# Kernel tuning notes

Hardware: AMD Instinct MI355X
Metric: run time of the kernel (lower is better)

Reference implementation:

```python
import jax, jax.numpy as jnp
import numpy as np

T, H, I, E = 512, 2048, 1408, 16
G, TOPK_GROUP, TOP_K = 4, 2, 6
RSF = 2.5  # routed_scaling_factor


def setup_inputs() -> dict:
    key = jax.random.key(0)
    ks = jax.random.split(key, 6)
    s = jnp.float32(0.02)
    return {
        "hidden_states": jax.random.normal(ks[0], (T, H), jnp.float32),
        "gate_weight": jax.random.normal(ks[1], (E, H), jnp.float32) * s,
        "correction_bias": jax.random.normal(ks[2], (E,), jnp.float32) * s,
        "w_gate": jax.random.normal(ks[3], (E, I, H), jnp.float32) * s,
        "w_up": jax.random.normal(ks[4], (E, I, H), jnp.float32) * s,
        "w_down": jax.random.normal(ks[5], (E, H, I), jnp.float32) * s,
    }


def _route(x, gate_weight, correction_bias):
    # MoEGate: logits = x @ W^T ; noaux_tc biased grouped top-k (sigmoid scoring)
    logits = x @ gate_weight.T                       # [T, E]
    scores = jax.nn.sigmoid(logits)                  # [T, E]
    sfc = scores + correction_bias                   # scores used for selection only
    # group score = sum of top-2 biased scores within each group
    gs = sfc.reshape(-1, G, E // G)                  # [T, G, E/G]
    group_scores = jax.lax.top_k(gs, 2)[0].sum(-1)   # [T, G]
    gidx = jax.lax.top_k(group_scores, TOPK_GROUP)[1]        # [T, topk_group]
    gmask = jnp.sum(jax.nn.one_hot(gidx, G, dtype=x.dtype), axis=1)  # [T, G]
    emask = jnp.repeat(gmask, E // G, axis=1)        # [T, E]
    masked = jnp.where(emask > 0, sfc, -jnp.inf)
    topk_idx = jax.lax.top_k(masked, TOP_K)[1]       # [T, K]
    # weights come from the UNbiased sigmoid scores
    topk_w = jnp.take_along_axis(scores, topk_idx, axis=1)   # [T, K]
    topk_w = topk_w / jnp.sum(topk_w, axis=-1, keepdims=True)  # renormalize
    topk_w = topk_w * jnp.asarray(RSF, x.dtype)      # routed_scaling_factor
    return topk_w, topk_idx


def _moe(x, topk_w, topk_idx, w_gate, w_up, w_down):
    # dispatch/grouped-GEMM/combine, expressed as a scan over experts with
    # per-token combine coefficients (same math as gather/grouped-GEMM/scatter)
    def step(acc, ws):
        wg, wu, wd, e = ws
        h = jax.nn.silu(x @ wg.T) * (x @ wu.T)       # [T, I] SiluAndMul
        out_e = h @ wd.T                             # [T, H]
        coef = jnp.sum(jnp.where(topk_idx == e, topk_w, 0.0), axis=1)  # [T]
        return acc + coef[:, None] * out_e, None

    acc0 = jnp.zeros_like(x)
    acc, _ = jax.lax.scan(step, acc0, (w_gate, w_up, w_down, jnp.arange(E)))
    return acc


def reference(hidden_states, gate_weight, correction_bias, w_gate, w_up, w_down):
    topk_w, topk_idx = _route(hidden_states, gate_weight, correction_bias)
    return _moe(hidden_states, topk_w, topk_idx, w_gate, w_up, w_down)
```

## Files before the change

### kernel.cpp

```cpp
#include <hip/hip_runtime.h>
#include <cstdint>

#define T_TOK 512
#define H_DIM 2048
#define I_DIM 1408
#define N_EXP 16

typedef __attribute__((ext_vector_type(8))) _Float16 f16x8;
typedef __attribute__((ext_vector_type(4))) float f32x4;

__device__ __forceinline__ void gload_lds16(const void* g, void* l) {
  auto gp = (const __attribute__((address_space(1))) unsigned int*)(unsigned long long)g;
  unsigned int loff = (unsigned int)(unsigned long long)l;
  auto lp = (__attribute__((address_space(3))) unsigned int*)loff;
  __builtin_amdgcn_global_load_lds(gp, lp, 16, 0, 0);
}

__device__ __forceinline__ f16x8 cvt8(f32x4 a, f32x4 b) {
  f16x8 r;
  r[0] = (_Float16)a[0]; r[1] = (_Float16)a[1]; r[2] = (_Float16)a[2]; r[3] = (_Float16)a[3];
  r[4] = (_Float16)b[0]; r[5] = (_Float16)b[1]; r[6] = (_Float16)b[2]; r[7] = (_Float16)b[3];
  return r;
}

__global__ __launch_bounds__(256) void route_kernel(
    const float* __restrict__ x, const float* __restrict__ gw,
    const float* __restrict__ bias, float* __restrict__ coef,
    _Float16* __restrict__ xb) {
  const int t = blockIdx.x;
  const int tid = threadIdx.x;
  const float* xt = x + (size_t)t * H_DIM;
  _Float16* xbt = xb + (size_t)t * H_DIM;

  float part[N_EXP];
#pragma unroll
  for (int e = 0; e < N_EXP; ++e) part[e] = 0.f;
  for (int j = tid; j < H_DIM; j += 256) {
    float xv = xt[j];
    xbt[j] = (_Float16)xv;
#pragma unroll
    for (int e = 0; e < N_EXP; ++e) part[e] += xv * gw[e * H_DIM + j];
  }
#pragma unroll
  for (int e = 0; e < N_EXP; ++e) {
#pragma unroll
    for (int off = 32; off > 0; off >>= 1) part[e] += __shfl_down(part[e], off);
  }
  __shared__ float red[4][N_EXP];
  const int lane = tid & 63, w = tid >> 6;
  if (lane == 0) {
#pragma unroll
    for (int e = 0; e < N_EXP; ++e) red[w][e] = part[e];
  }
  __syncthreads();
  if (tid == 0) {
    float s[16], sf[16];
    for (int e = 0; e < 16; ++e) {
      float lg = red[0][e] + red[1][e] + red[2][e] + red[3][e];
      s[e] = 1.f / (1.f + expf(-lg));
      sf[e] = s[e] + bias[e];
    }
    float gsc[4];
    for (int g = 0; g < 4; ++g) {
      float m1 = -1e30f, m2 = -1e30f;
      for (int j = 0; j < 4; ++j) {
        float v = sf[g * 4 + j];
        if (v > m1) { m2 = m1; m1 = v; }
        else if (v > m2) { m2 = v; }
      }
      gsc[g] = m1 + m2;
    }
    int g1 = 0;
    for (int g = 1; g < 4; ++g) if (gsc[g] > gsc[g1]) g1 = g;
    int g2 = -1;
    for (int g = 0; g < 4; ++g) {
      if (g == g1) continue;
      if (g2 < 0 || gsc[g] > gsc[g2]) g2 = g;
    }
    bool gok[4];
    for (int g = 0; g < 4; ++g) gok[g] = (g == g1) || (g == g2);
    bool sel[16];
    for (int e = 0; e < 16; ++e) sel[e] = false;
    float wsum = 0.f;
    for (int k = 0; k < 6; ++k) {
      int best = -1; float bv = 0.f;
      for (int e2 = 0; e2 < 16; ++e2) {
        if (!gok[e2 >> 2] || sel[e2]) continue;
        if (best < 0 || sf[e2] > bv) { bv = sf[e2]; best = e2; }
      }
      sel[best] = true;
      wsum += s[best];
    }
    float inv = 2.5f / wsum;
    for (int e = 0; e < 16; ++e) coef[t * N_EXP + e] = sel[e] ? s[e] * inv : 0.f;
  }
}

__global__ __launch_bounds__(512) void build_lists_kernel(
    const float* __restrict__ coef, int* __restrict__ counts,
    int* __restrict__ lists) {
  const int e = blockIdx.x;
  const int t = threadIdx.x;
  const bool flag = coef[t * N_EXP + e] != 0.f;
  const unsigned long long m = __ballot(flag);
  const int lane = t & 63, w = t >> 6;
  __shared__ int wcnt[8], woff[8];
  if (lane == 0) wcnt[w] = __popcll(m);
  __syncthreads();
  if (t == 0) {
    int a = 0;
    for (int i = 0; i < 8; ++i) { woff[i] = a; a += wcnt[i]; }
    counts[e] = a;
  }
  __syncthreads();
  if (flag) {
    int pos = woff[w] + __popcll(m & ((1ull << lane) - 1ull));
    lists[e * T_TOK + pos] = t;
  }
}

__global__ __launch_bounds__(512) void gate_up_kernel(
    const _Float16* __restrict__ xb, const float* __restrict__ wg,
    const float* __restrict__ wu, const int* __restrict__ counts,
    const int* __restrict__ lists, _Float16* __restrict__ hbuf) {
  extern __shared__ char lds[];
  const int e = blockIdx.z;
  const int ne = counts[e];
  const int row0 = blockIdx.y * 256;
  if (row0 >= ne) return;
  const int col0 = blockIdx.x * 64;
  const int tid = threadIdx.x;
  const int lane = tid & 63;
  const int w = tid >> 6;
  const int wr = w >> 1, wc = w & 1;

  const int* lst = lists + e * T_TOK;
  const _Float16* asrc[4];
#pragma unroll
  for (int i = 0; i < 4; ++i) {
    int tr = (w * 4 + i) * 8 + (lane >> 3);
    int tok = lst[min(row0 + tr, ne - 1)];
    int lchunk = (lane & 7) ^ (tr & 7);
    asrc[i] = xb + (size_t)tok * H_DIM + lchunk * 8;
  }
  const float* bgs[2];
  const float* bus[2];
#pragma unroll
  for (int i = 0; i < 2; ++i) {
    int tr = (w * 2 + i) * 4 + (lane >> 4);
    int ls = (lane & 15) ^ ((tr & 7) << 1);
    bgs[i] = wg + ((size_t)e * I_DIM + col0 + tr) * H_DIM + ls * 4;
    bus[i] = wu + ((size_t)e * I_DIM + col0 + tr) * H_DIM + ls * 4;
  }

  f32x4 accg[4][2], accu[4][2];
  const f32x4 zz = {0.f, 0.f, 0.f, 0.f};
#pragma unroll
  for (int m = 0; m < 4; ++m)
#pragma unroll
    for (int n = 0; n < 2; ++n) { accg[m][n] = zz; accu[m][n] = zz; }

  auto stage = [&](int kt, int buf) {
    const int k0 = kt * 64;
#pragma unroll
    for (int i = 0; i < 4; ++i)
      gload_lds16(asrc[i] + k0, lds + buf * 32768 + (w * 4 + i) * 1024);
#pragma unroll
    for (int i = 0; i < 2; ++i) {
      gload_lds16(bgs[i] + k0, lds + 65536 + buf * 16384 + (w * 2 + i) * 1024);
      gload_lds16(bus[i] + k0, lds + 98304 + buf * 16384 + (w * 2 + i) * 1024);
    }
  };

  auto comp = [&](int buf) {
    const char* Ab = lds + buf * 32768;
    const char* Gb = lds + 65536 + buf * 16384;
    const char* Ub = lds + 98304 + buf * 16384;
#pragma unroll
    for (int kk = 0; kk < 2; ++kk) {
      f16x8 afr[4], bg[2], bu[2];
#pragma unroll
      for (int m = 0; m < 4; ++m) {
        int row = wr * 64 + m * 16 + (lane & 15);
        int pch = (kk * 4 + (lane >> 4)) ^ (row & 7);
        afr[m] = *(const f16x8*)(Ab + row * 128 + pch * 16);
      }
#pragma unroll
      for (int n = 0; n < 2; ++n) {
        int c = wc * 32 + n * 16 + (lane & 15);
        int s0 = kk * 8 + (lane >> 4) * 2;
        int p0 = s0 ^ ((c & 7) << 1);
        int p1 = (s0 + 1) ^ ((c & 7) << 1);
        bg[n] = cvt8(*(const f32x4*)(Gb + c * 256 + p0 * 16),
                     *(const f32x4*)(Gb + c * 256 + p1 * 16));
        bu[n] = cvt8(*(const f32x4*)(Ub + c * 256 + p0 * 16),
                     *(const f32x4*)(Ub + c * 256 + p1 * 16));
      }
#pragma unroll
      for (int m = 0; m < 4; ++m)
#pragma unroll
        for (int n = 0; n < 2; ++n) {
          accg[m][n] = __builtin_amdgcn_mfma_f32_16x16x32_f16(afr[m], bg[n], accg[m][n], 0, 0, 0);
          accu[m][n] = __builtin_amdgcn_mfma_f32_16x16x32_f16(afr[m], bu[n], accu[m][n], 0, 0, 0);
        }
    }
  };

  const int NK = H_DIM / 64;
  stage(0, 0);
  for (int kt = 0; kt < NK; ++kt) {
    __syncthreads();
    if (kt + 1 < NK) stage(kt + 1, (kt + 1) & 1);
    comp(kt & 1);
  }

  _Float16* hb = hbuf + (size_t)e * T_TOK * I_DIM;
#pragma unroll
  for (int m = 0; m < 4; ++m) {
#pragma unroll
    for (int j = 0; j < 4; ++j) {
      int r = row0 + wr * 64 + m * 16 + (lane >> 4) * 4 + j;
      if (r < ne) {
#pragma unroll
        for (int n = 0; n < 2; ++n) {
          int cc = col0 + wc * 32 + n * 16 + (lane & 15);
          float g = accg[m][n][j];
          float u = accu[m][n][j];
          float hv = (g / (1.f + __expf(-g))) * u;
          hb[(size_t)r * I_DIM + cc] = (_Float16)hv;
        }
      }
    }
  }
}

__global__ __launch_bounds__(512) void down_kernel(
    const _Float16* __restrict__ hbuf, const float* __restrict__ wd,
    const int* __restrict__ counts, const int* __restrict__ lists,
    const float* __restrict__ coef, float* __restrict__ out) {
  extern __shared__ char lds[];
  const int e = blockIdx.z;
  const int ne = counts[e];
  const int row0 = blockIdx.y * 256;
  if (row0 >= ne) return;
  const int col0 = blockIdx.x * 64;
  const int tid = threadIdx.x;
  const int lane = tid & 63;
  const int w = tid >> 6;
  const int wr = w >> 1, wc = w & 1;

  const _Float16* hb = hbuf + (size_t)e * T_TOK * I_DIM;
  const _Float16* asrc[4];
#pragma unroll
  for (int i = 0; i < 4; ++i) {
    int tr = (w * 4 + i) * 8 + (lane >> 3);
    int lchunk = (lane & 7) ^ (tr & 7);
    asrc[i] = hb + (size_t)(row0 + tr) * I_DIM + lchunk * 8;
  }
  const float* bds[2];
#pragma unroll
  for (int i = 0; i < 2; ++i) {
    int tr = (w * 2 + i) * 4 + (lane >> 4);
    int ls = (lane & 15) ^ ((tr & 7) << 1);
    bds[i] = wd + ((size_t)e * H_DIM + col0 + tr) * I_DIM + ls * 4;
  }

  f32x4 acc[4][2];
  const f32x4 zz = {0.f, 0.f, 0.f, 0.f};
#pragma unroll
  for (int m = 0; m < 4; ++m)
#pragma unroll
    for (int n = 0; n < 2; ++n) acc[m][n] = zz;

  auto stage = [&](int kt, int buf) {
    const int k0 = kt * 64;
#pragma unroll
    for (int i = 0; i < 4; ++i)
      gload_lds16(asrc[i] + k0, lds + buf * 32768 + (w * 4 + i) * 1024);
#pragma unroll
    for (int i = 0; i < 2; ++i)
      gload_lds16(bds[i] + k0, lds + 65536 + buf * 16384 + (w * 2 + i) * 1024);
  };

  auto comp = [&](int buf) {
    const char* Ab = lds + buf * 32768;
    const char* Bb = lds + 65536 + buf * 16384;
#pragma unroll
    for (int kk = 0; kk < 2; ++kk) {
      f16x8 afr[4], bf[2];
#pragma unroll
      for (int m = 0; m < 4; ++m) {
        int row = wr * 64 + m * 16 + (lane & 15);
        int pch = (kk * 4 + (lane >> 4)) ^ (row & 7);
        afr[m] = *(const f16x8*)(Ab + row * 128 + pch * 16);
      }
#pragma unroll
      for (int n = 0; n < 2; ++n) {
        int c = wc * 32 + n * 16 + (lane & 15);
        int s0 = kk * 8 + (lane >> 4) * 2;
        int p0 = s0 ^ ((c & 7) << 1);
        int p1 = (s0 + 1) ^ ((c & 7) << 1);
        bf[n] = cvt8(*(const f32x4*)(Bb + c * 256 + p0 * 16),
                     *(const f32x4*)(Bb + c * 256 + p1 * 16));
      }
#pragma unroll
      for (int m = 0; m < 4; ++m)
#pragma unroll
        for (int n = 0; n < 2; ++n)
          acc[m][n] = __builtin_amdgcn_mfma_f32_16x16x32_f16(afr[m], bf[n], acc[m][n], 0, 0, 0);
    }
  };

  const int NK = I_DIM / 64;
  stage(0, 0);
  for (int kt = 0; kt < NK; ++kt) {
    __syncthreads();
    if (kt + 1 < NK) stage(kt + 1, (kt + 1) & 1);
    comp(kt & 1);
  }

#pragma unroll
  for (int m = 0; m < 4; ++m) {
#pragma unroll
    for (int j = 0; j < 4; ++j) {
      int r = row0 + wr * 64 + m * 16 + (lane >> 4) * 4 + j;
      if (r < ne) {
        int tok = lists[e * T_TOK + r];
        float c = coef[tok * N_EXP + e];
#pragma unroll
        for (int n = 0; n < 2; ++n) {
          int cc = col0 + wc * 32 + n * 16 + (lane & 15);
          atomicAdd(&out[(size_t)tok * H_DIM + cc], acc[m][n][j] * c);
        }
      }
    }
  }
}

extern "C" void kernel_launch(void* const* d_in, const int* in_sizes, int n_in,
                              void* d_out, int out_size, void* d_ws, size_t ws_size,
                              hipStream_t stream) {
  const float* x  = (const float*)d_in[0];
  const float* gw = (const float*)d_in[1];
  const float* cb = (const float*)d_in[2];
  const float* wg = (const float*)d_in[3];
  const float* wu = (const float*)d_in[4];
  const float* wd = (const float*)d_in[5];
  float* out = (float*)d_out;
  char* ws = (char*)d_ws;

  float* coef   = (float*)(ws);
  int*   counts = (int*)(ws + 32768);
  int*   lists  = (int*)(ws + 33024);
  _Float16* xb  = (_Float16*)(ws + 66048);
  _Float16* hbuf= (_Float16*)(ws + 66048 + 2097152 + 256);

  hipFuncSetAttribute((const void*)gate_up_kernel,
                      hipFuncAttributeMaxDynamicSharedMemorySize, 131072);
  hipFuncSetAttribute((const void*)down_kernel,
                      hipFuncAttributeMaxDynamicSharedMemorySize, 98304);

  hipMemsetAsync(d_out, 0, (size_t)out_size * sizeof(float), stream);

  route_kernel<<<T_TOK, 256, 0, stream>>>(x, gw, cb, coef, xb);
  build_lists_kernel<<<N_EXP, 512, 0, stream>>>(coef, counts, lists);
  gate_up_kernel<<<dim3(I_DIM / 64, 2, N_EXP), 512, 131072, stream>>>(xb, wg, wu, counts, lists, hbuf);
  down_kernel<<<dim3(H_DIM / 64, 2, N_EXP), 512, 98304, stream>>>(hbuf, wd, counts, lists, coef, out);
}
```

Baseline: 213.1 us.

## Shrink gate_up tile to 128 rows and K=32 with static LDS

```diff
diff --git a/kernel.cpp b/kernel.cpp
--- a/kernel.cpp
+++ b/kernel.cpp
@@ -119,14 +119,14 @@
   }
 }
 
-__global__ __launch_bounds__(512) void gate_up_kernel(
+__global__ __launch_bounds__(256) void gate_up_kernel(
     const _Float16* __restrict__ xb, const float* __restrict__ wg,
     const float* __restrict__ wu, const int* __restrict__ counts,
     const int* __restrict__ lists, _Float16* __restrict__ hbuf) {
-  extern __shared__ char lds[];
+  __shared__ char lds[49152];
   const int e = blockIdx.z;
   const int ne = counts[e];
-  const int row0 = blockIdx.y * 256;
+  const int row0 = blockIdx.y * 128;
   if (row0 >= ne) return;
   const int col0 = blockIdx.x * 64;
   const int tid = threadIdx.x;
@@ -135,20 +135,19 @@
   const int wr = w >> 1, wc = w & 1;
 
   const int* lst = lists + e * T_TOK;
-  const _Float16* asrc[4];
-#pragma unroll
-  for (int i = 0; i < 4; ++i) {
-    int tr = (w * 4 + i) * 8 + (lane >> 3);
-    int tok = lst[min(row0 + tr, ne - 1)];
-    int lchunk = (lane & 7) ^ (tr & 7);
-    asrc[i] = xb + (size_t)tok * H_DIM + lchunk * 8;
+  const _Float16* asrc[2];
+#pragma unroll
+  for (int i = 0; i < 2; ++i) {
+    int r = row0 + (2 * w + i) * 16 + (lane & 15);
+    int tok = lst[min(r, ne - 1)];
+    asrc[i] = xb + (size_t)tok * H_DIM + (lane >> 4) * 8;
   }
   const float* bgs[2];
   const float* bus[2];
 #pragma unroll
   for (int i = 0; i < 2; ++i) {
-    int tr = (w * 2 + i) * 4 + (lane >> 4);
-    int ls = (lane & 15) ^ ((tr & 7) << 1);
+    int tr = (w * 2 + i) * 8 + (lane >> 3);
+    int ls = (lane & 7) ^ (tr & 7);
     bgs[i] = wg + ((size_t)e * I_DIM + col0 + tr) * H_DIM + ls * 4;
     bus[i] = wu + ((size_t)e * I_DIM + col0 + tr) * H_DIM + ls * 4;
   }
@@ -161,52 +160,46 @@
     for (int n = 0; n < 2; ++n) { accg[m][n] = zz; accu[m][n] = zz; }
 
   auto stage = [&](int kt, int buf) {
-    const int k0 = kt * 64;
-#pragma unroll
-    for (int i = 0; i < 4; ++i)
-      gload_lds16(asrc[i] + k0, lds + buf * 32768 + (w * 4 + i) * 1024);
+    const int k0 = kt * 32;
+#pragma unroll
+    for (int i = 0; i < 2; ++i)
+      gload_lds16(asrc[i] + k0, lds + buf * 8192 + (2 * w + i) * 1024);
 #pragma unroll
     for (int i = 0; i < 2; ++i) {
-      gload_lds16(bgs[i] + k0, lds + 65536 + buf * 16384 + (w * 2 + i) * 1024);
-      gload_lds16(bus[i] + k0, lds + 98304 + buf * 16384 + (w * 2 + i) * 1024);
+      gload_lds16(bgs[i] + k0, lds + 16384 + buf * 8192 + (w * 2 + i) * 1024);
+      gload_lds16(bus[i] + k0, lds + 32768 + buf * 8192 + (w * 2 + i) * 1024);
     }
   };
 
   auto comp = [&](int buf) {
-    const char* Ab = lds + buf * 32768;
-    const char* Gb = lds + 65536 + buf * 16384;
-    const char* Ub = lds + 98304 + buf * 16384;
-#pragma unroll
-    for (int kk = 0; kk < 2; ++kk) {
-      f16x8 afr[4], bg[2], bu[2];
-#pragma unroll
-      for (int m = 0; m < 4; ++m) {
-        int row = wr * 64 + m * 16 + (lane & 15);
-        int pch = (kk * 4 + (lane >> 4)) ^ (row & 7);
-        afr[m] = *(const f16x8*)(Ab + row * 128 + pch * 16);
-      }
+    const char* Ab = lds + buf * 8192;
+    const char* Gb = lds + 16384 + buf * 8192;
+    const char* Ub = lds + 32768 + buf * 8192;
+    f16x8 afr[4], bg[2], bu[2];
+#pragma unroll
+    for (int m = 0; m < 4; ++m)
+      afr[m] = *(const f16x8*)(Ab + (wr * 4 + m) * 1024 + lane * 16);
+    const int s0 = (lane >> 4) * 2;
+#pragma unroll
+    for (int n = 0; n < 2; ++n) {
+      int c = wc * 32 + n * 16 + (lane & 15);
+      int p0 = s0 ^ (c & 7);
+      int p1 = (s0 + 1) ^ (c & 7);
+      bg[n] = cvt8(*(const f32x4*)(Gb + c * 128 + p0 * 16),
+                   *(const f32x4*)(Gb + c * 128 + p1 * 16));
+      bu[n] = cvt8(*(const f32x4*)(Ub + c * 128 + p0 * 16),
+                   *(const f32x4*)(Ub + c * 128 + p1 * 16));
+    }
+#pragma unroll
+    for (int m = 0; m < 4; ++m)
 #pragma unroll
       for (int n = 0; n < 2; ++n) {
-        int c = wc * 32 + n * 16 + (lane & 15);
-        int s0 = kk * 8 + (lane >> 4) * 2;
-        int p0 = s0 ^ ((c & 7) << 1);
-        int p1 = (s0 + 1) ^ ((c & 7) << 1);
-        bg[n] = cvt8(*(const f32x4*)(Gb + c * 256 + p0 * 16),
-                     *(const f32x4*)(Gb + c * 256 + p1 * 16));
-        bu[n] = cvt8(*(const f32x4*)(Ub + c * 256 + p0 * 16),
-                     *(const f32x4*)(Ub + c * 256 + p1 * 16));
-      }
-#pragma unroll
-      for (int m = 0; m < 4; ++m)
-#pragma unroll
-        for (int n = 0; n < 2; ++n) {
-          accg[m][n] = __builtin_amdgcn_mfma_f32_16x16x32_f16(afr[m], bg[n], accg[m][n], 0, 0, 0);
-          accu[m][n] = __builtin_amdgcn_mfma_f32_16x16x32_f16(afr[m], bu[n], accu[m][n], 0, 0, 0);
-        }
-    }
+        accg[m][n] = __builtin_amdgcn_mfma_f32_16x16x32_f16(afr[m], bg[n], accg[m][n], 0, 0, 0);
+        accu[m][n] = __builtin_amdgcn_mfma_f32_16x16x32_f16(afr[m], bu[n], accu[m][n], 0, 0, 0);
+      }
   };
 
-  const int NK = H_DIM / 64;
+  const int NK = H_DIM / 32;
   stage(0, 0);
   for (int kt = 0; kt < NK; ++kt) {
     __syncthreads();
@@ -355,8 +348,6 @@
   _Float16* xb  = (_Float16*)(ws + 66048);
   _Float16* hbuf= (_Float16*)(ws + 66048 + 2097152 + 256);
 
-  hipFuncSetAttribute((const void*)gate_up_kernel,
-                      hipFuncAttributeMaxDynamicSharedMemorySize, 131072);
   hipFuncSetAttribute((const void*)down_kernel,
                       hipFuncAttributeMaxDynamicSharedMemorySize, 98304);
 
@@ -364,6 +355,6 @@
 
   route_kernel<<<T_TOK, 256, 0, stream>>>(x, gw, cb, coef, xb);
   build_lists_kernel<<<N_EXP, 512, 0, stream>>>(coef, counts, lists);
-  gate_up_kernel<<<dim3(I_DIM / 64, 2, N_EXP), 512, 131072, stream>>>(xb, wg, wu, counts, lists, hbuf);
+  gate_up_kernel<<<dim3(I_DIM / 64, 4, N_EXP), 256, 0, stream>>>(xb, wg, wu, counts, lists, hbuf);
   down_kernel<<<dim3(H_DIM / 64, 2, N_EXP), 512, 98304, stream>>>(hbuf, wd, counts, lists, coef, out);
 }
```

New measurement: 245.3 us. 15.1% more time.
